# Performance work log

Measured on AMD Instinct MI355X. Metric: run time of the kernel, lower is better.

Reference implementation:

```python
import jax, jax.numpy as jnp
import numpy as np
from jax import lax

# Surrogate spike: forward = Heaviside, backward = g / (1 + 5|x|)^2
@jax.custom_vjp
def spike_fn(x):
    return (x >= 0).astype(x.dtype)

def _spk_fwd(x):
    return spike_fn(x), x

def _spk_bwd(x, g):
    return (g / (1.0 + 5.0 * jnp.abs(x)) ** 2,)

spike_fn.defvjp(_spk_fwd, _spk_bwd)

BN_EPS = 1e-5

def _batchnorm(x, scale, bias, mean, var):
    # x: (B, C, T); eval-mode BN with running stats
    inv = scale / jnp.sqrt(var + BN_EPS)
    return x * inv[None, :, None] + (bias - mean * inv)[None, :, None]

def _conv1d(x, w, b, pad):
    y = lax.conv_general_dilated(x, w, (1,), [(pad, pad)],
                                 dimension_numbers=('NCH', 'OIH', 'NCH'))
    return y + b[None, :, None]

def setup_inputs() -> dict:
    key = jax.random.key(0)
    ks = jax.random.split(key, 12)
    B, T, EEG, GEO, TH, H, OUT = 4096, 320, 64, 18, 32, 16, 4
    inp = {
        'x_eeg': jax.random.normal(ks[0], (B, T, EEG), jnp.float32),
        'x_geo': jax.random.normal(ks[1], (B, T, GEO), jnp.float32),
        'conv1_w': jax.random.normal(ks[2], (TH, EEG, 5), jnp.float32) * 0.05,
        'conv1_b': jnp.zeros((TH,), jnp.float32),
        'bn1_s': jnp.ones((TH,), jnp.float32),
        'bn1_b': jnp.zeros((TH,), jnp.float32),
        'bn1_m': jnp.zeros((TH,), jnp.float32),
        'bn1_v': jnp.ones((TH,), jnp.float32),
        'conv2_w': jax.random.normal(ks[3], (H, TH, 3), jnp.float32) * 0.1,
        'conv2_b': jnp.zeros((H,), jnp.float32),
        'bn2_s': jnp.ones((H,), jnp.float32),
        'bn2_b': jnp.zeros((H,), jnp.float32),
        'bn2_m': jnp.zeros((H,), jnp.float32),
        'bn2_v': jnp.ones((H,), jnp.float32),
        'geo_w': jax.random.normal(ks[4], (H, GEO), jnp.float32) * 0.2,
        'geo_b': jnp.zeros((H,), jnp.float32),
        'gamma': jnp.full((H,), 0.5, jnp.float32),
        'fc1_w': jax.random.normal(ks[5], (64, 160), jnp.float32) * 0.08,
        'fc1_b': jnp.zeros((64,), jnp.float32),
        'fc2_w': jax.random.normal(ks[6], (OUT, 64), jnp.float32) * 0.12,
        'fc2_b': jnp.zeros((OUT,), jnp.float32),
    }
    return inp

def reference(x_eeg, x_geo, conv1_w, conv1_b, bn1_s, bn1_b, bn1_m, bn1_v,
              conv2_w, conv2_b, bn2_s, bn2_b, bn2_m, bn2_v,
              geo_w, geo_b, gamma, fc1_w, fc1_b, fc2_w, fc2_b):
    B, T, _ = x_eeg.shape
    theta_0, beta, tau_a, tau_m = 0.5, 1.8, 0.36, 0.8

    # EEG temporal encoder (eval mode: dropout = identity)
    h = x_eeg.transpose(0, 2, 1)  # (B, 64, T)
    h = jax.nn.relu(_batchnorm(_conv1d(h, conv1_w, conv1_b, 2), bn1_s, bn1_b, bn1_m, bn1_v))
    h = jax.nn.relu(_batchnorm(_conv1d(h, conv2_w, conv2_b, 1), bn2_s, bn2_b, bn2_m, bn2_v))
    eeg_encoded = h.transpose(0, 2, 1)  # (B, T, 16)

    geo_mod = jax.nn.sigmoid(jnp.einsum('bti,hi->bth', x_geo, geo_w) + geo_b)  # (B, T, 16)

    H = eeg_encoded.shape[-1]
    zeros = jnp.zeros((B, H), x_eeg.dtype)
    init = (zeros, zeros, zeros, zeros)  # mem_alif, eta, mem_li, prev_spk

    def step(carry, xs):
        mem_alif, eta, mem_li, prev_spk = carry
        cur_eeg, cur_geo = xs
        eta = tau_a * eta + (1.0 - tau_a) * prev_spk
        theta_t = theta_0 + beta * eta - gamma * cur_geo
        mem_alif = tau_m * mem_alif + cur_eeg
        spk = spike_fn(mem_alif - theta_t)
        mem_alif = mem_alif * (1.0 - spk)
        mem_li = 0.9 * mem_li + spk
        return (mem_alif, eta, mem_li, spk), mem_li

    xs = (eeg_encoded.transpose(1, 0, 2), geo_mod.transpose(1, 0, 2))  # (T, B, 16)
    _, pot = lax.scan(step, init, xs)  # (T, B, 16)

    pot = pot.transpose(1, 2, 0)                 # (B, 16, T)
    windows = pot.reshape(B, H, 10, 32)          # T = 320 = 10*32
    dp_feat = (windows[..., 16:].mean(-1) - windows[..., :16].mean(-1)).reshape(B, -1)  # (B, 160)

    out = jax.nn.relu(dp_feat @ fc1_w.T + fc1_b) @ fc2_w.T + fc2_b  # (B, 4)
    return out
```

## Files before the change

### kernel.cpp

```cpp
#include <hip/hip_runtime.h>
#include <math.h>

#define TB    4096
#define TSEQ  320
#define NEEG  64
#define NTH   32
#define NH    16
#define NGEO  18
#define TILE_T 64
#define NTILES 5
#define XROWS2 70
#define H1ROWS 66

typedef _Float16 f16x8 __attribute__((ext_vector_type(8)));
typedef _Float16 f16x2 __attribute__((ext_vector_type(2)));
typedef float f32x4 __attribute__((ext_vector_type(4)));
#define INV2048 4.8828125e-4f

#define OFF_W1F  0
#define OFF_W2F  10240
#define OFF_B1   11776
#define OFF_B2   11808
#define OFF_GWT  11824
#define OFF_FC1T 12112
#define OFF_FC2T 22352
#define OFF_ZP   22656
#define OFF_E    32768
#define SZ_EC    (TB*TSEQ*NH)
#define OFF_C    (OFF_E + SZ_EC)
#define OFF_DP   (OFF_C + SZ_EC)
#define SZ_DP    (TB*160)
#define REQ_FLOATS ((size_t)OFF_DP + SZ_DP)
#define REQ_BYTES  (REQ_FLOATS * 4)

__global__ void __launch_bounds__(256)
prep_kernel(const float* __restrict__ c1w, const float* __restrict__ c1b,
            const float* __restrict__ s1,  const float* __restrict__ bb1,
            const float* __restrict__ mm1, const float* __restrict__ vv1,
            const float* __restrict__ c2w, const float* __restrict__ c2b,
            const float* __restrict__ s2,  const float* __restrict__ bb2,
            const float* __restrict__ mm2, const float* __restrict__ vv2,
            const float* __restrict__ gw,  const float* __restrict__ fc1w,
            const float* __restrict__ fc2w, float* __restrict__ ws)
{
    const int tid = threadIdx.x;
    _Float16* w1fp = reinterpret_cast<_Float16*>(ws + OFF_W1F);
    _Float16* w2fp = reinterpret_cast<_Float16*>(ws + OFF_W2F);

    for (int d = tid; d < 10240; d += 256) {
        int j = d & 7, l = (d >> 3) & 63, nbk = d >> 9;
        int kk = nbk >> 1, nb = nbk & 1;
        int k = kk >> 1, i = (kk & 1) * 32 + ((l >> 4) * 8) + j;
        int c = nb * 16 + (l & 15);
        float inv = s1[c] / sqrtf(vv1[c] + 1e-5f);
        float wv = c1w[c * 320 + i * 5 + k] * inv;
        _Float16 hi = (_Float16)wv;
        _Float16 lo = (_Float16)((wv - (float)hi) * 2048.f);
        w1fp[((nbk * 2 + 0) * 64 + l) * 8 + j] = hi;
        w1fp[((nbk * 2 + 1) * 64 + l) * 8 + j] = lo;
    }
    for (int d = tid; d < 1536; d += 256) {
        int j = d & 7, l = (d >> 3) & 63, kk2 = d >> 9;
        int c = (l >> 4) * 8 + j;
        int o = l & 15;
        float inv = s2[o] / sqrtf(vv2[o] + 1e-5f);
        float wv = c2w[o * 96 + c * 3 + kk2] * inv;
        _Float16 hi = (_Float16)wv;
        _Float16 lo = (_Float16)((wv - (float)hi) * 2048.f);
        w2fp[((kk2 * 2 + 0) * 64 + l) * 8 + j] = hi;
        w2fp[((kk2 * 2 + 1) * 64 + l) * 8 + j] = lo;
    }
    if (tid < NTH) {
        float inv = s1[tid] / sqrtf(vv1[tid] + 1e-5f);
        ws[OFF_B1 + tid] = c1b[tid] * inv + bb1[tid] - mm1[tid] * inv;
    }
    if (tid < NH) {
        float inv = s2[tid] / sqrtf(vv2[tid] + 1e-5f);
        ws[OFF_B2 + tid] = c2b[tid] * inv + bb2[tid] - mm2[tid] * inv;
    }
    for (int d = tid; d < NGEO * NH; d += 256) {
        int i = d / NH, h = d - i * NH;
        ws[OFF_GWT + d] = gw[h * NGEO + i];
    }
    for (int d = tid; d < 160 * 64; d += 256) {
        int f = d / 64, o = d - f * 64;
        ws[OFF_FC1T + d] = fc1w[o * 160 + f];
    }
    if (tid < 256) {
        int j = tid / 4, o = tid - j * 4;
        ws[OFF_FC2T + tid] = fc2w[o * 64 + j];
    }
    if (tid < 64) ws[OFF_ZP + tid] = 0.f;
}

__global__ void __launch_bounds__(256, 2)
convm_kernel(const float* __restrict__ xeeg, const float* __restrict__ xgeo,
             const float* __restrict__ ws,   const float* __restrict__ geo_b,
             const float* __restrict__ gamma,
             float* __restrict__ E, float* __restrict__ C)
{
    __shared__ __align__(16) float xbuf[2][XROWS2 * 64];
    __shared__ __align__(16) float xg32[18 * 64];
    __shared__ __align__(16) _Float16 h1h[H1ROWS * 32];
    __shared__ __align__(16) _Float16 h1l[H1ROWS * 32];
    __shared__ __align__(16) float gws[NGEO * NH];
    __shared__ float b1s[32], b2s[16], gbs[16], gams[16];

    const int b = blockIdx.x, tid = threadIdx.x;
    const int l = tid & 63, w = tid >> 6;
    const int lrow = l & 15, lkg = l >> 4;
    const int nb = w >> 1, wsub = w & 1;
    const int ug = tid >> 2, hq = tid & 3;

    const float* xb  = xeeg + (size_t)b * TSEQ * NEEG;
    const float* xgb = xgeo + (size_t)b * TSEQ * NGEO;
    const float* zp  = ws + OFF_ZP;

#define STAGE_DMA(buf, t0n) do {                                                     \
        for (int c_ = w; c_ < XROWS2; c_ += 4) {                                     \
            int tg_ = (t0n) - 3 + c_;                                                \
            const float* s_ = (tg_ >= 0 && tg_ < TSEQ)                               \
                              ? (xb + (size_t)tg_ * 64 + l) : zp;                    \
            __builtin_amdgcn_global_load_lds(                                        \
                (const __attribute__((address_space(1))) void*)s_,                   \
                (__attribute__((address_space(3))) void*)&xbuf[(buf)][c_ * 64],      \
                4, 0, 0);                                                            \
        }                                                                            \
        for (int c_ = w; c_ < 18; c_ += 4) {                                         \
            const float* s_ = xgb + (size_t)(t0n) * NGEO + c_ * 64 + l;              \
            __builtin_amdgcn_global_load_lds(                                        \
                (const __attribute__((address_space(1))) void*)s_,                   \
                (__attribute__((address_space(3))) void*)&xg32[c_ * 64],             \
                4, 0, 0);                                                            \
        }                                                                            \
    } while (0)

    f16x8 B1h[10], B1l[10], B2h[3], B2l[3];
    {
        const f16x8* wsrc = reinterpret_cast<const f16x8*>(ws + OFF_W1F);
        #pragma unroll
        for (int kk = 0; kk < 10; ++kk) {
            B1h[kk] = wsrc[((kk * 2 + nb) * 2 + 0) * 64 + l];
            B1l[kk] = wsrc[((kk * 2 + nb) * 2 + 1) * 64 + l];
        }
        const f16x8* wsrc2 = reinterpret_cast<const f16x8*>(ws + OFF_W2F);
        #pragma unroll
        for (int kk = 0; kk < 3; ++kk) {
            B2h[kk] = wsrc2[(kk * 2 + 0) * 64 + l];
            B2l[kk] = wsrc2[(kk * 2 + 1) * 64 + l];
        }
    }
    {
        if (tid < 32) b1s[tid] = ws[OFF_B1 + tid];
        if (tid < 16) {
            b2s[tid] = ws[OFF_B2 + tid];
            gbs[tid] = geo_b[tid];
            gams[tid] = gamma[tid];
        }
        for (int p = tid; p < NGEO * NH; p += 256) gws[p] = ws[OFF_GWT + p];
    }
    STAGE_DMA(0, 0);
    __syncthreads();

    for (int jt = 0; jt < NTILES; ++jt) {
        const int t0 = jt * TILE_T;
        const int cur = jt & 1;
        _Float16* xh = reinterpret_cast<_Float16*>(&xbuf[cur][0]);
        _Float16* xl = xh + XROWS2 * 64;

        float2 xr2[9];
        #pragma unroll
        for (int q = 0; q < 9; ++q) {
            int p = tid + q * 256;
            if (p < 2240) {
                int xr = p >> 5, ip = (p & 31) * 2;
                xr2[q] = *reinterpret_cast<const float2*>(&xbuf[cur][xr * 64 + ip]);
            }
        }
        {
            float z0 = gbs[hq * 4 + 0], z1 = gbs[hq * 4 + 1];
            float z2 = gbs[hq * 4 + 2], z3 = gbs[hq * 4 + 3];
            const float* xgr = &xg32[ug * NGEO];
            #pragma unroll
            for (int ii = 0; ii < NGEO; ++ii) {
                float xv = xgr[ii];
                float4 wv = *reinterpret_cast<const float4*>(&gws[ii * 16 + hq * 4]);
                z0 = fmaf(xv, wv.x, z0);
                z1 = fmaf(xv, wv.y, z1);
                z2 = fmaf(xv, wv.z, z2);
                z3 = fmaf(xv, wv.w, z3);
            }
            const int t4o = (t0 + ug) >> 2, tt = ug & 3;
            float* cp = C + (((size_t)t4o * TB + b) * 16 + hq * 4) * 4 + tt;
            cp[0]  = gams[hq * 4 + 0] * (1.f / (1.f + expf(-z0)));
            cp[4]  = gams[hq * 4 + 1] * (1.f / (1.f + expf(-z1)));
            cp[8]  = gams[hq * 4 + 2] * (1.f / (1.f + expf(-z2)));
            cp[12] = gams[hq * 4 + 3] * (1.f / (1.f + expf(-z3)));
        }
        __syncthreads();

        #pragma unroll
        for (int q = 0; q < 9; ++q) {
            int p = tid + q * 256;
            if (p < 2240) {
                int xr = p >> 5, ip = (p & 31) * 2;
                float f0 = xr2[q].x, f1 = xr2[q].y;
                _Float16 h0 = (_Float16)f0, h1v = (_Float16)f1;
                f16x2 vh = {h0, h1v};
                f16x2 vl = {(_Float16)((f0 - (float)h0) * 2048.f),
                            (_Float16)((f1 - (float)h1v) * 2048.f)};
                int idx = xr * 64 + (((ip >> 3) ^ (xr & 7)) << 3) + (ip & 7);
                *reinterpret_cast<f16x2*>(&xh[idx]) = vh;
                *reinterpret_cast<f16x2*>(&xl[idx]) = vl;
            }
        }
        __syncthreads();

        if (jt + 1 < NTILES) STAGE_DMA(cur ^ 1, (jt + 1) * TILE_T);
        __builtin_amdgcn_s_setprio(1);
        {
            const float bia = b1s[nb * 16 + lrow];
            #pragma unroll
            for (int pi = 0; pi < 3; ++pi) {
                if (pi == 2 && ((jt & 1) != wsub)) break;
                const int mb = (pi < 2) ? (wsub + pi * 2) : 4;
                const int mbase = mb * 16;
                int s = mbase + lrow; if (s > 65) s = 65;
                f32x4 aH = {0.f, 0.f, 0.f, 0.f};
                f32x4 aM = aH, aL = aH;
                #pragma unroll
                for (int kk = 0; kk < 10; ++kk) {
                    const int xr = s + (kk >> 1);
                    const int gx = (kk & 1) * 4 + lkg;
                    const int off = xr * 64 + ((gx ^ (xr & 7)) << 3);
                    f16x8 Ah = *reinterpret_cast<const f16x8*>(&xh[off]);
                    f16x8 Al = *reinterpret_cast<const f16x8*>(&xl[off]);
                    aH = __builtin_amdgcn_mfma_f32_16x16x32_f16(Ah, B1h[kk], aH, 0, 0, 0);
                    aM = __builtin_amdgcn_mfma_f32_16x16x32_f16(Ah, B1l[kk], aM, 0, 0, 0);
                    aL = __builtin_amdgcn_mfma_f32_16x16x32_f16(Al, B1h[kk], aL, 0, 0, 0);
                }
                #pragma unroll
                for (int r = 0; r < 4; ++r) {
                    int so = mbase + lkg * 4 + r;
                    if (so < 66) {
                        int tg = t0 - 1 + so;
                        bool v = (tg >= 0 && tg < TSEQ);
                        float val = v ? fmaxf(fmaf(aM[r] + aL[r], INV2048, aH[r]) + bia, 0.f) : 0.f;
                        int key = (so >> 1) & 3;
                        int g = (nb * 2 + (lrow >> 3)) ^ key;
                        int idx = so * 32 + (g << 3) + (lrow & 7);
                        _Float16 hh = (_Float16)val;
                        h1h[idx] = hh;
                        h1l[idx] = (_Float16)((val - (float)hh) * 2048.f);
                    }
                }
            }
        }
        __builtin_amdgcn_s_setprio(0);
        __syncthreads();

        {
            const int ub = w * 16;
            f32x4 aH = {0.f, 0.f, 0.f, 0.f};
            f32x4 aM = aH, aL = aH;
            __builtin_amdgcn_s_setprio(1);
            #pragma unroll
            for (int kk = 0; kk < 3; ++kk) {
                int srow = ub + lrow + kk;
                int off = srow * 32 + ((lkg ^ ((srow >> 1) & 3)) << 3);
                f16x8 Ah = *reinterpret_cast<const f16x8*>(&h1h[off]);
                f16x8 Al = *reinterpret_cast<const f16x8*>(&h1l[off]);
                aH = __builtin_amdgcn_mfma_f32_16x16x32_f16(Ah, B2h[kk], aH, 0, 0, 0);
                aM = __builtin_amdgcn_mfma_f32_16x16x32_f16(Ah, B2l[kk], aM, 0, 0, 0);
                aL = __builtin_amdgcn_mfma_f32_16x16x32_f16(Al, B2h[kk], aL, 0, 0, 0);
            }
            __builtin_amdgcn_s_setprio(0);
            const float bia = b2s[lrow];
            float4 ev;
            float* evp = reinterpret_cast<float*>(&ev);
            #pragma unroll
            for (int r = 0; r < 4; ++r)
                evp[r] = fmaxf(fmaf(aM[r] + aL[r], INV2048, aH[r]) + bia, 0.f);
            const int t4o = ((t0 + ub) >> 2) + lkg;
            float* ep = E + (((size_t)t4o * TB + b) * 16 + lrow) * 4;
            *reinterpret_cast<float4*>(ep) = ev;
        }
    }
#undef STAGE_DMA
}

__global__ void __launch_bounds__(256)
scan_kernel(const float* __restrict__ E, const float* __restrict__ C,
            float* __restrict__ DP)
{
    const int tid = threadIdx.x;
    const int h = tid & 15;
    const int b = blockIdx.x * 16 + (tid >> 4);
    const float4* e4 = reinterpret_cast<const float4*>(E);
    const float4* c4 = reinterpret_cast<const float4*>(C);
    const size_t idx = (size_t)b * 16 + h;
    const size_t slab = (size_t)TB * 16;

    float eta = 0.f, memv = 0.f, li = 0.f, ps = 0.f, accF = 0.f, accS = 0.f;
    float4 ev = e4[idx], cv = c4[idx];
    for (int t4 = 0; t4 < 80; ++t4) {
        float4 en, cn;
        if (t4 < 79) { en = e4[(size_t)(t4 + 1) * slab + idx]; cn = c4[(size_t)(t4 + 1) * slab + idx]; }
        const float* evp = reinterpret_cast<const float*>(&ev);
        const float* cvp = reinterpret_cast<const float*>(&cv);
        #pragma unroll
        for (int tt = 0; tt < 4; ++tt) {
            float e = evp[tt], c = cvp[tt];
            eta = 0.36f * eta + 0.64f * ps;
            float theta = 0.5f + 1.8f * eta - c;
            memv = 0.8f * memv + e;
            float spk = (memv - theta >= 0.f) ? 1.f : 0.f;
            memv *= (1.f - spk);
            li = 0.9f * li + spk;
            ps = spk;
            int t = t4 * 4 + tt;
            if (((t >> 4) & 1) == 0) accF += li; else accS += li;
        }
        if ((t4 & 7) == 7) {
            DP[(size_t)b * 160 + h * 10 + (t4 >> 3)] = (accS - accF) * 0.0625f;
            accF = 0.f; accS = 0.f;
        }
        ev = en; cv = cn;
    }
}

__global__ void __launch_bounds__(256)
fc_kernel(const float* __restrict__ DP, const float* __restrict__ ws,
          const float* __restrict__ fc1_b, const float* __restrict__ fc2_b,
          float* __restrict__ out)
{
    __shared__ float sh_dp[4][160];
    __shared__ float mid[4][64];
    const int tid = threadIdx.x;
    const int b0 = blockIdx.x * 4;
    for (int p = tid; p < 640; p += 256)
        sh_dp[p / 160][p - (p / 160) * 160] = DP[(size_t)b0 * 160 + p];
    __syncthreads();
    {
        const int bl = tid >> 6, o = tid & 63;
        const float* __restrict__ fc1t = ws + OFF_FC1T;
        float z = fc1_b[o];
        for (int f = 0; f < 160; ++f) z = fmaf(sh_dp[bl][f], fc1t[f * 64 + o], z);
        mid[bl][o] = fmaxf(z, 0.f);
    }
    __syncthreads();
    if (tid < 16) {
        const int bl = tid >> 2, oo = tid & 3;
        const float* __restrict__ fc2t = ws + OFF_FC2T;
        float z = fc2_b[oo];
        #pragma unroll
        for (int jj = 0; jj < 64; ++jj) z = fmaf(mid[bl][jj], fc2t[jj * 4 + oo], z);
        out[(size_t)(b0 + bl) * 4 + oo] = z;
    }
}

extern "C" void kernel_launch(void* const* d_in, const int* in_sizes, int n_in,
                              void* d_out, int out_size, void* d_ws, size_t ws_size,
                              hipStream_t stream)
{
    const float* xeeg = (const float*)d_in[0];
    const float* xgeo = (const float*)d_in[1];
    const float* c1w  = (const float*)d_in[2];
    const float* c1b  = (const float*)d_in[3];
    const float* s1   = (const float*)d_in[4];
    const float* bb1  = (const float*)d_in[5];
    const float* mm1  = (const float*)d_in[6];
    const float* vv1  = (const float*)d_in[7];
    const float* c2w  = (const float*)d_in[8];
    const float* c2b  = (const float*)d_in[9];
    const float* s2   = (const float*)d_in[10];
    const float* bb2  = (const float*)d_in[11];
    const float* mm2  = (const float*)d_in[12];
    const float* vv2  = (const float*)d_in[13];
    const float* gw   = (const float*)d_in[14];
    const float* gb   = (const float*)d_in[15];
    const float* gam  = (const float*)d_in[16];
    const float* fc1w = (const float*)d_in[17];
    const float* fc1b = (const float*)d_in[18];
    const float* fc2w = (const float*)d_in[19];
    const float* fc2b = (const float*)d_in[20];
    float* ws   = (float*)d_ws;
    float* outp = (float*)d_out;

    hipLaunchKernelGGL(prep_kernel, dim3(1), dim3(256), 0, stream,
                       c1w, c1b, s1, bb1, mm1, vv1, c2w, c2b, s2, bb2, mm2, vv2,
                       gw, fc1w, fc2w, ws);

    float* E  = ws + OFF_E;
    float* C  = ws + OFF_C;
    float* DP = ws + OFF_DP;
    hipLaunchKernelGGL(convm_kernel, dim3(TB), dim3(256), 0, stream,
                       xeeg, xgeo, ws, gb, gam, E, C);
    hipLaunchKernelGGL(scan_kernel, dim3(TB / 16), dim3(256), 0, stream,
                       E, C, DP);
    hipLaunchKernelGGL(fc_kernel, dim3(TB / 4), dim3(256), 0, stream,
                       DP, ws, fc1b, fc2b, outp);
}
```

Baseline: 310.5 us.

## Move geo sigmoid modulation into scan kernel and fuse FC head

Measured after the change: 445.2 us. 43.3% more time.

```diff
diff --git a/kernel.cpp b/kernel.cpp
--- a/kernel.cpp
+++ b/kernel.cpp
@@ -26,12 +26,6 @@
 #define OFF_FC2T 22352
 #define OFF_ZP   22656
 #define OFF_E    32768
-#define SZ_EC    (TB*TSEQ*NH)
-#define OFF_C    (OFF_E + SZ_EC)
-#define OFF_DP   (OFF_C + SZ_EC)
-#define SZ_DP    (TB*160)
-#define REQ_FLOATS ((size_t)OFF_DP + SZ_DP)
-#define REQ_BYTES  (REQ_FLOATS * 4)
 
 __global__ void __launch_bounds__(256)
 prep_kernel(const float* __restrict__ c1w, const float* __restrict__ c1b,
@@ -94,27 +88,21 @@
 }
 
 __global__ void __launch_bounds__(256, 2)
-convm_kernel(const float* __restrict__ xeeg, const float* __restrict__ xgeo,
-             const float* __restrict__ ws,   const float* __restrict__ geo_b,
-             const float* __restrict__ gamma,
-             float* __restrict__ E, float* __restrict__ C)
+convm_kernel(const float* __restrict__ xeeg, const float* __restrict__ ws,
+             float* __restrict__ E)
 {
     __shared__ __align__(16) float xbuf[2][XROWS2 * 64];
-    __shared__ __align__(16) float xg32[18 * 64];
     __shared__ __align__(16) _Float16 h1h[H1ROWS * 32];
     __shared__ __align__(16) _Float16 h1l[H1ROWS * 32];
-    __shared__ __align__(16) float gws[NGEO * NH];
-    __shared__ float b1s[32], b2s[16], gbs[16], gams[16];
+    __shared__ float b1s[32], b2s[16];
 
     const int b = blockIdx.x, tid = threadIdx.x;
     const int l = tid & 63, w = tid >> 6;
     const int lrow = l & 15, lkg = l >> 4;
     const int nb = w >> 1, wsub = w & 1;
-    const int ug = tid >> 2, hq = tid & 3;
-
-    const float* xb  = xeeg + (size_t)b * TSEQ * NEEG;
-    const float* xgb = xgeo + (size_t)b * TSEQ * NGEO;
-    const float* zp  = ws + OFF_ZP;
+
+    const float* xb = xeeg + (size_t)b * TSEQ * NEEG;
+    const float* zp = ws + OFF_ZP;
 
 #define STAGE_DMA(buf, t0n) do {                                                     \
         for (int c_ = w; c_ < XROWS2; c_ += 4) {                                     \
@@ -126,13 +114,6 @@
                 (__attribute__((address_space(3))) void*)&xbuf[(buf)][c_ * 64],      \
                 4, 0, 0);                                                            \
         }                                                                            \
-        for (int c_ = w; c_ < 18; c_ += 4) {                                         \
-            const float* s_ = xgb + (size_t)(t0n) * NGEO + c_ * 64 + l;              \
-            __builtin_amdgcn_global_load_lds(                                        \
-                (const __attribute__((address_space(1))) void*)s_,                   \
-                (__attribute__((address_space(3))) void*)&xg32[c_ * 64],             \
-                4, 0, 0);                                                            \
-        }                                                                            \
     } while (0)
 
     f16x8 B1h[10], B1l[10], B2h[3], B2l[3];
@@ -150,15 +131,9 @@
             B2l[kk] = wsrc2[(kk * 2 + 1) * 64 + l];
         }
     }
-    {
-        if (tid < 32) b1s[tid] = ws[OFF_B1 + tid];
-        if (tid < 16) {
-            b2s[tid] = ws[OFF_B2 + tid];
-            gbs[tid] = geo_b[tid];
-            gams[tid] = gamma[tid];
-        }
-        for (int p = tid; p < NGEO * NH; p += 256) gws[p] = ws[OFF_GWT + p];
-    }
+    if (tid < 32) b1s[tid] = ws[OFF_B1 + tid];
+    if (tid < 16) b2s[tid] = ws[OFF_B2 + tid];
+
     STAGE_DMA(0, 0);
     __syncthreads();
 
@@ -176,26 +151,6 @@
                 int xr = p >> 5, ip = (p & 31) * 2;
                 xr2[q] = *reinterpret_cast<const float2*>(&xbuf[cur][xr * 64 + ip]);
             }
-        }
-        {
-            float z0 = gbs[hq * 4 + 0], z1 = gbs[hq * 4 + 1];
-            float z2 = gbs[hq * 4 + 2], z3 = gbs[hq * 4 + 3];
-            const float* xgr = &xg32[ug * NGEO];
-            #pragma unroll
-            for (int ii = 0; ii < NGEO; ++ii) {
-                float xv = xgr[ii];
-                float4 wv = *reinterpret_cast<const float4*>(&gws[ii * 16 + hq * 4]);
-                z0 = fmaf(xv, wv.x, z0);
-                z1 = fmaf(xv, wv.y, z1);
-                z2 = fmaf(xv, wv.z, z2);
-                z3 = fmaf(xv, wv.w, z3);
-            }
-            const int t4o = (t0 + ug) >> 2, tt = ug & 3;
-            float* cp = C + (((size_t)t4o * TB + b) * 16 + hq * 4) * 4 + tt;
-            cp[0]  = gams[hq * 4 + 0] * (1.f / (1.f + expf(-z0)));
-            cp[4]  = gams[hq * 4 + 1] * (1.f / (1.f + expf(-z1)));
-            cp[8]  = gams[hq * 4 + 2] * (1.f / (1.f + expf(-z2)));
-            cp[12] = gams[hq * 4 + 3] * (1.f / (1.f + expf(-z3)));
         }
         __syncthreads();
 
@@ -289,28 +244,67 @@
 #undef STAGE_DMA
 }
 
-__global__ void __launch_bounds__(256)
-scan_kernel(const float* __restrict__ E, const float* __restrict__ C,
-            float* __restrict__ DP)
+__global__ void __launch_bounds__(64)
+scanfc_kernel(const float* __restrict__ E, const float* __restrict__ xgeo,
+              const float* __restrict__ ws, const float* __restrict__ geo_b,
+              const float* __restrict__ gamma, const float* __restrict__ fc1_b,
+              const float* __restrict__ fc2_b, float* __restrict__ out)
 {
+    __shared__ float gws_l[NGEO * NH];
+    __shared__ float gb_l[16], gam_l[16];
+    __shared__ float xgs[2][4][72];
+    __shared__ float dp_lds[4][160];
+    __shared__ float mid[4][64];
+
     const int tid = threadIdx.x;
-    const int h = tid & 15;
-    const int b = blockIdx.x * 16 + (tid >> 4);
+    const int h = tid & 15, bl = tid >> 4;
+    const int b0 = blockIdx.x * 4;
+    const int b = b0 + bl;
+
+    for (int p = tid; p < NGEO * NH; p += 64) gws_l[p] = ws[OFF_GWT + p];
+    if (tid < 16) { gb_l[tid] = geo_b[tid]; gam_l[tid] = gamma[tid]; }
+
     const float4* e4 = reinterpret_cast<const float4*>(E);
-    const float4* c4 = reinterpret_cast<const float4*>(C);
+    const size_t slab = (size_t)TB * 16;
     const size_t idx = (size_t)b * 16 + h;
-    const size_t slab = (size_t)TB * 16;
-
+
+    #pragma unroll
+    for (int k = 0; k < 5; ++k) {
+        int p = tid + k * 64;
+        if (p < 288) {
+            int bb = p / 72, r = p - bb * 72;
+            xgs[0][bb][r] = xgeo[(size_t)(b0 + bb) * TSEQ * NGEO + r];
+        }
+    }
+    float4 ev = e4[idx];
     float eta = 0.f, memv = 0.f, li = 0.f, ps = 0.f, accF = 0.f, accS = 0.f;
-    float4 ev = e4[idx], cv = c4[idx];
+
     for (int t4 = 0; t4 < 80; ++t4) {
-        float4 en, cn;
-        if (t4 < 79) { en = e4[(size_t)(t4 + 1) * slab + idx]; cn = c4[(size_t)(t4 + 1) * slab + idx]; }
+        const int cur = t4 & 1;
+        __syncthreads();
+        if (t4 < 79) {
+            #pragma unroll
+            for (int k = 0; k < 5; ++k) {
+                int p = tid + k * 64;
+                if (p < 288) {
+                    int bb = p / 72, r = p - bb * 72;
+                    xgs[cur ^ 1][bb][r] =
+                        xgeo[((size_t)(b0 + bb) * TSEQ + (size_t)(t4 + 1) * 4) * NGEO + r];
+                }
+            }
+        }
+        float4 en;
+        if (t4 < 79) en = e4[(size_t)(t4 + 1) * slab + idx];
         const float* evp = reinterpret_cast<const float*>(&ev);
-        const float* cvp = reinterpret_cast<const float*>(&cv);
         #pragma unroll
         for (int tt = 0; tt < 4; ++tt) {
-            float e = evp[tt], c = cvp[tt];
+            float z = gb_l[h];
+            const float* xr = &xgs[cur][bl][tt * 18];
+            #pragma unroll
+            for (int ii = 0; ii < NGEO; ++ii)
+                z = fmaf(xr[ii], gws_l[ii * 16 + h], z);
+            float c = gam_l[h] * (1.f / (1.f + expf(-z)));
+            float e = evp[tt];
             eta = 0.36f * eta + 0.64f * ps;
             float theta = 0.5f + 1.8f * eta - c;
             memv = 0.8f * memv + e;
@@ -322,40 +316,34 @@
             if (((t >> 4) & 1) == 0) accF += li; else accS += li;
         }
         if ((t4 & 7) == 7) {
-            DP[(size_t)b * 160 + h * 10 + (t4 >> 3)] = (accS - accF) * 0.0625f;
+            dp_lds[bl][h * 10 + (t4 >> 3)] = (accS - accF) * 0.0625f;
             accF = 0.f; accS = 0.f;
         }
-        ev = en; cv = cn;
-    }
-}
-
-__global__ void __launch_bounds__(256)
-fc_kernel(const float* __restrict__ DP, const float* __restrict__ ws,
-          const float* __restrict__ fc1_b, const float* __restrict__ fc2_b,
-          float* __restrict__ out)
-{
-    __shared__ float sh_dp[4][160];
-    __shared__ float mid[4][64];
-    const int tid = threadIdx.x;
-    const int b0 = blockIdx.x * 4;
-    for (int p = tid; p < 640; p += 256)
-        sh_dp[p / 160][p - (p / 160) * 160] = DP[(size_t)b0 * 160 + p];
+        ev = en;
+    }
     __syncthreads();
+
     {
-        const int bl = tid >> 6, o = tid & 63;
         const float* __restrict__ fc1t = ws + OFF_FC1T;
-        float z = fc1_b[o];
-        for (int f = 0; f < 160; ++f) z = fmaf(sh_dp[bl][f], fc1t[f * 64 + o], z);
-        mid[bl][o] = fmaxf(z, 0.f);
+        #pragma unroll
+        for (int k = 0; k < 4; ++k) {
+            int id = tid + k * 64;
+            int bb = id >> 6, o = id & 63;
+            float z = fc1_b[o];
+            for (int f = 0; f < 160; ++f)
+                z = fmaf(dp_lds[bb][f], fc1t[f * 64 + o], z);
+            mid[bb][o] = fmaxf(z, 0.f);
+        }
     }
     __syncthreads();
     if (tid < 16) {
-        const int bl = tid >> 2, oo = tid & 3;
         const float* __restrict__ fc2t = ws + OFF_FC2T;
+        int bb = tid >> 2, oo = tid & 3;
         float z = fc2_b[oo];
         #pragma unroll
-        for (int jj = 0; jj < 64; ++jj) z = fmaf(mid[bl][jj], fc2t[jj * 4 + oo], z);
-        out[(size_t)(b0 + bl) * 4 + oo] = z;
+        for (int jj = 0; jj < 64; ++jj)
+            z = fmaf(mid[bb][jj], fc2t[jj * 4 + oo], z);
+        out[(size_t)(b0 + bb) * 4 + oo] = z;
     }
 }
 
@@ -391,13 +379,9 @@
                        c1w, c1b, s1, bb1, mm1, vv1, c2w, c2b, s2, bb2, mm2, vv2,
                        gw, fc1w, fc2w, ws);
 
-    float* E  = ws + OFF_E;
-    float* C  = ws + OFF_C;
-    float* DP = ws + OFF_DP;
+    float* E = ws + OFF_E;
     hipLaunchKernelGGL(convm_kernel, dim3(TB), dim3(256), 0, stream,
-                       xeeg, xgeo, ws, gb, gam, E, C);
-    hipLaunchKernelGGL(scan_kernel, dim3(TB / 16), dim3(256), 0, stream,
-                       E, C, DP);
-    hipLaunchKernelGGL(fc_kernel, dim3(TB / 4), dim3(256), 0, stream,
-                       DP, ws, fc1b, fc2b, outp);
+                       xeeg, ws, E);
+    hipLaunchKernelGGL(scanfc_kernel, dim3(TB / 4), dim3(64), 0, stream,
+                       E, xgeo, ws, gb, gam, fc1b, fc2b, outp);
 }
```
